# Kernel optimization log

Hardware: AMD Instinct MI355X
Metric: run time of the kernel (lower is better)

Reference implementation:

```python
import jax, jax.numpy as jnp
import numpy as np

N_CHANNELS = 29
HIDDEN = [5, 4, 4]
IN_FEAT = 7
OUT_FEAT = 3
EPS = 1e-07


def _glorot(key, fan_in, fan_out, shape):
    lim = np.sqrt(6.0 / (fan_in + fan_out))
    return jax.random.uniform(key, shape, jnp.float32, -lim, lim)


def _make_params(key):
    # Batched per-channel weights: stack n_channels tiny MLPs along leading dim.
    sizes = [IN_FEAT] + HIDDEN + [OUT_FEAT]
    Ws, bs = [], []
    for i in range(len(sizes) - 1):
        key, k = jax.random.split(key)
        Ws.append(_glorot(k, sizes[i], sizes[i + 1], (N_CHANNELS, sizes[i], sizes[i + 1])))
        bs.append(jnp.zeros((N_CHANNELS, sizes[i + 1]), jnp.float32))
    return Ws, bs


def setup_inputs() -> dict:
    key = jax.random.key(0)
    ks = jax.random.split(key, 16)
    N = 262144
    inp = {
        "tau": jax.random.uniform(ks[0], (N, N_CHANNELS, 1), jnp.float32),
        "mu": jax.random.uniform(ks[1], (N, 1), jnp.float32, 0.05, 1.0),
        "mu_bar": jax.random.uniform(ks[2], (N, 1), jnp.float32, 0.05, 1.0),
        "lw": jax.random.uniform(ks[3], (N, 1), jnp.float32),
        "h2o": jax.random.uniform(ks[4], (N, 1), jnp.float32),
        "o3": jax.random.uniform(ks[5], (N, 1), jnp.float32),
        "co2": jax.random.uniform(ks[6], (N, 1), jnp.float32),
        "u": jax.random.uniform(ks[7], (N, 1), jnp.float32),
        "n2o": jax.random.uniform(ks[8], (N, 1), jnp.float32),
        "ch4": jax.random.uniform(ks[9], (N, 1), jnp.float32),
    }
    Wd, bd = _make_params(ks[10])
    Wf, bf = _make_params(ks[11])
    for i in range(4):
        inp[f"Wd{i}"] = Wd[i]
        inp[f"bd{i}"] = bd[i]
        inp[f"Wf{i}"] = Wf[i]
        inp[f"bf{i}"] = bf[i]
    return inp


def _mlp(x, Ws, bs):
    # x: [N, F]; Ws[i]: [C, fin, fout]; output [N, C, 3]
    h = jnp.einsum('nf,cfh->nch', x, Ws[0]) + bs[0]
    h = jax.nn.relu(h)
    for i in (1, 2):
        h = jnp.einsum('nch,chk->nck', h, Ws[i]) + bs[i]
        h = jax.nn.relu(h)
    h = jnp.einsum('nch,chk->nck', h, Ws[3]) + bs[3]
    return jax.nn.softmax(h, axis=-1)


def reference(tau, mu, mu_bar, lw, h2o, o3, co2, u, n2o, ch4,
              Wd0, bd0, Wd1, bd1, Wd2, bd2, Wd3, bd3,
              Wf0, bf0, Wf1, bf1, Wf2, bf2, Wf3, bf3):
    constituents = jnp.concatenate([lw, h2o, o3, co2, u, n2o, ch4], axis=1)  # [N,7]
    c_direct = constituents / (mu + EPS)
    c_diffuse = constituents / (mu_bar + EPS)
    mu3 = mu[:, :, None]          # [N,1,1]
    mu_bar3 = mu_bar[:, :, None]
    tau_total = jnp.sum(tau, axis=-1, keepdims=True)  # [N,C,1]
    t_direct = jnp.exp(-tau_total / (mu3 + EPS))       # [N,C,1]
    t_diffuse = jnp.exp(-tau_total / (mu_bar3 + EPS))
    e_direct = _mlp(c_direct, [Wd0, Wd1, Wd2, Wd3], [bd0, bd1, bd2, bd3])    # [N,C,3]
    e_diffuse = _mlp(c_diffuse, [Wf0, Wf1, Wf2, Wf3], [bf0, bf1, bf2, bf3])  # [N,C,3]
    return jnp.concatenate([t_direct, t_diffuse, e_direct, e_diffuse], axis=2)  # [N,C,8]
```

## Files before the change

### kernel.cpp

```cpp
#include <hip/hip_runtime.h>

#define EPS 1e-7f
#define NCH 29
#define SPB 128
#define ROWF4 59


typedef float f32x2 __attribute__((ext_vector_type(2)));

__device__ __forceinline__ f32x2 splat2(float v) { f32x2 r; r.x = v; r.y = v; return r; }
__device__ __forceinline__ f32x2 fma2(f32x2 a, f32x2 b, f32x2 c) {
    return __builtin_elementwise_fma(a, b, c);
}
__device__ __forceinline__ f32x2 max2(f32x2 a, f32x2 b) {
    return __builtin_elementwise_max(a, b);
}
__device__ __forceinline__ f32x2 expc2(f32x2 a) {
    f32x2 r; r.x = __expf(a.x); r.y = __expf(a.y); return r;
}
__device__ __forceinline__ f32x2 rcp2(f32x2 a) {
    f32x2 r; r.x = __builtin_amdgcn_rcpf(a.x); r.y = __builtin_amdgcn_rcpf(a.y); return r;
}

__device__ __forceinline__ void barrier_lds_only() {
    asm volatile("s_waitcnt lgkmcnt(0)\n\ts_barrier" ::: "memory");
}

__device__ __forceinline__ void mlp7p(const f32x2 x[7],
    const float* __restrict__ W0, const float* __restrict__ b0,
    const float* __restrict__ W1, const float* __restrict__ b1,
    const float* __restrict__ W2, const float* __restrict__ b2,
    const float* __restrict__ W3, const float* __restrict__ b3,
    f32x2 e[3])
{
    const f32x2 zero = splat2(0.0f);
    f32x2 h0[5];
#pragma unroll
    for (int h = 0; h < 5; ++h) {
        f32x2 a = splat2(b0[h]);
#pragma unroll
        for (int f = 0; f < 7; ++f) a = fma2(x[f], splat2(W0[f * 5 + h]), a);
        h0[h] = max2(a, zero);
    }
    f32x2 h1[4];
#pragma unroll
    for (int k = 0; k < 4; ++k) {
        f32x2 a = splat2(b1[k]);
#pragma unroll
        for (int h = 0; h < 5; ++h) a = fma2(h0[h], splat2(W1[h * 4 + k]), a);
        h1[k] = max2(a, zero);
    }
    f32x2 h2[4];
#pragma unroll
    for (int k = 0; k < 4; ++k) {
        f32x2 a = splat2(b2[k]);
#pragma unroll
        for (int h = 0; h < 4; ++h) a = fma2(h1[h], splat2(W2[h * 4 + k]), a);
        h2[k] = max2(a, zero);
    }
    f32x2 l[3];
#pragma unroll
    for (int k = 0; k < 3; ++k) {
        f32x2 a = splat2(b3[k]);
#pragma unroll
        for (int h = 0; h < 4; ++h) a = fma2(h2[h], splat2(W3[h * 3 + k]), a);
        l[k] = a;
    }
    f32x2 m = max2(l[0], max2(l[1], l[2]));
    f32x2 e0 = expc2(l[0] - m);
    f32x2 e1 = expc2(l[1] - m);
    f32x2 e2 = expc2(l[2] - m);
    f32x2 rs = rcp2(e0 + e1 + e2);
    e[0] = e0 * rs; e[1] = e1 * rs; e[2] = e2 * rs;
}

__global__ __launch_bounds__(512, 4) void lps_kernel(
    const float* __restrict__ tau, const float* __restrict__ mu, const float* __restrict__ mu_bar,
    const float* __restrict__ lw, const float* __restrict__ h2o, const float* __restrict__ o3,
    const float* __restrict__ co2, const float* __restrict__ uu, const float* __restrict__ n2o,
    const float* __restrict__ ch4,
    const float* __restrict__ Wd0, const float* __restrict__ bd0,
    const float* __restrict__ Wf0, const float* __restrict__ bf0,
    const float* __restrict__ Wd1, const float* __restrict__ bd1,
    const float* __restrict__ Wf1, const float* __restrict__ bf1,
    const float* __restrict__ Wd2, const float* __restrict__ bd2,
    const float* __restrict__ Wf2, const float* __restrict__ bf2,
    const float* __restrict__ Wd3, const float* __restrict__ bd3,
    const float* __restrict__ Wf3, const float* __restrict__ bf3,
    float* __restrict__ out, int N)
{
    __shared__ __align__(16) float4 obuf[64 * ROWF4];

    const int tid  = threadIdx.x;
    const int lane = tid & 63;
    const int wid  = __builtin_amdgcn_readfirstlane(tid >> 6);

    const long long base = (long long)blockIdx.x * SPB;
    const int s0 = (int)base + lane;
    const int s1 = s0 + 64;
    const int i0 = (s0 < N) ? s0 : (N - 1);
    const int i1 = (s1 < N) ? s1 : (N - 1);

    f32x2 mu2, mub2;
    mu2.x  = mu[i0];      mu2.y  = mu[i1];
    mub2.x = mu_bar[i0];  mub2.y = mu_bar[i1];
    const f32x2 rmu2   = rcp2(mu2 + splat2(EPS));
    const f32x2 rmub2  = rcp2(mub2 + splat2(EPS));
    const f32x2 nrmu2  = -rmu2;
    const f32x2 nrmub2 = -rmub2;

    f32x2 cons2[7];
    cons2[0].x = lw[i0];  cons2[0].y = lw[i1];
    cons2[1].x = h2o[i0]; cons2[1].y = h2o[i1];
    cons2[2].x = o3[i0];  cons2[2].y = o3[i1];
    cons2[3].x = co2[i0]; cons2[3].y = co2[i1];
    cons2[4].x = uu[i0];  cons2[4].y = uu[i1];
    cons2[5].x = n2o[i0]; cons2[5].y = n2o[i1];
    cons2[6].x = ch4[i0]; cons2[6].y = ch4[i1];

    f32x2 x2d[7], x2f[7];
#pragma unroll
    for (int f = 0; f < 7; ++f) { x2d[f] = cons2[f] * rmu2; x2f[f] = cons2[f] * rmub2; }

    float ry[4][8];

#pragma unroll
    for (int it = 0; it < 4; ++it) {
        const int c = wid + it * 8;
        if (c < NCH) {
            f32x2 tau2;
            tau2.x = tau[(size_t)i0 * NCH + c];
            tau2.y = tau[(size_t)i1 * NCH + c];
            f32x2 td2 = expc2(tau2 * nrmu2);
            f32x2 tf2 = expc2(tau2 * nrmub2);

            f32x2 ed[3], ef[3];
            mlp7p(x2d, Wd0 + c * 35, bd0 + c * 5, Wd1 + c * 20, bd1 + c * 4,
                       Wd2 + c * 16, bd2 + c * 4, Wd3 + c * 12, bd3 + c * 3, ed);
            mlp7p(x2f, Wf0 + c * 35, bf0 + c * 5, Wf1 + c * 20, bf1 + c * 4,
                       Wf2 + c * 16, bf2 + c * 4, Wf3 + c * 12, bf3 + c * 3, ef);

            obuf[lane * ROWF4 + c * 2]     = make_float4(td2.x, tf2.x, ed[0].x, ed[1].x);
            obuf[lane * ROWF4 + c * 2 + 1] = make_float4(ed[2].x, ef[0].x, ef[1].x, ef[2].x);
            ry[it][0] = td2.y;   ry[it][1] = tf2.y;
            ry[it][2] = ed[0].y; ry[it][3] = ed[1].y;
            ry[it][4] = ed[2].y; ry[it][5] = ef[0].y;
            ry[it][6] = ef[1].y; ry[it][7] = ef[2].y;
        }
    }

    float4* out4 = (float4*)out;

    barrier_lds_only();
    {
        int n0 = N - (int)base; n0 = (n0 > 64) ? 64 : n0;
        if (n0 > 0) {
            const int tot = n0 * 58;
            const long long ob = base * 58;
            for (int i = tid; i < tot; i += 512) {
                const int s = i / 58, r = i - s * 58;
                out4[ob + i] = obuf[s * ROWF4 + r];
            }
        }
    }
    barrier_lds_only();

#pragma unroll
    for (int it = 0; it < 4; ++it) {
        const int c = wid + it * 8;
        if (c < NCH) {
            obuf[lane * ROWF4 + c * 2]     = make_float4(ry[it][0], ry[it][1], ry[it][2], ry[it][3]);
            obuf[lane * ROWF4 + c * 2 + 1] = make_float4(ry[it][4], ry[it][5], ry[it][6], ry[it][7]);
        }
    }
    barrier_lds_only();

    {
        int n1 = N - (int)base - 64; n1 = (n1 > 64) ? 64 : n1;
        if (n1 > 0) {
            const int tot = n1 * 58;
            const long long ob = (base + 64) * 58;
            for (int i = tid; i < tot; i += 512) {
                const int s = i / 58, r = i - s * 58;
                out4[ob + i] = obuf[s * ROWF4 + r];
            }
        }
    }
}

extern "C" void kernel_launch(void* const* d_in, const int* in_sizes, int n_in,
                              void* d_out, int out_size, void* d_ws, size_t ws_size,
                              hipStream_t stream) {
    const float* tau    = (const float*)d_in[0];
    const float* mu     = (const float*)d_in[1];
    const float* mu_bar = (const float*)d_in[2];
    const float* lw     = (const float*)d_in[3];
    const float* h2o    = (const float*)d_in[4];
    const float* o3     = (const float*)d_in[5];
    const float* co2    = (const float*)d_in[6];
    const float* uu     = (const float*)d_in[7];
    const float* n2o    = (const float*)d_in[8];
    const float* ch4    = (const float*)d_in[9];

    const float* Wd0 = (const float*)d_in[10];
    const float* bd0 = (const float*)d_in[11];
    const float* Wf0 = (const float*)d_in[12];
    const float* bf0 = (const float*)d_in[13];
    const float* Wd1 = (const float*)d_in[14];
    const float* bd1 = (const float*)d_in[15];
    const float* Wf1 = (const float*)d_in[16];
    const float* bf1 = (const float*)d_in[17];
    const float* Wd2 = (const float*)d_in[18];
    const float* bd2 = (const float*)d_in[19];
    const float* Wf2 = (const float*)d_in[20];
    const float* bf2 = (const float*)d_in[21];
    const float* Wd3 = (const float*)d_in[22];
    const float* bd3 = (const float*)d_in[23];
    const float* Wf3 = (const float*)d_in[24];
    const float* bf3 = (const float*)d_in[25];

    float* out = (float*)d_out;
    int N = in_sizes[1];

    int blocks = (N + SPB - 1) / SPB;
    lps_kernel<<<blocks, 512, 0, stream>>>(
        tau, mu, mu_bar, lw, h2o, o3, co2, uu, n2o, ch4,
        Wd0, bd0, Wf0, bf0, Wd1, bd1, Wf1, bf1,
        Wd2, bd2, Wf2, bf2, Wd3, bd3, Wf3, bf3,
        out, N);
}
```

Measured before the change: 82.72 us.

## Stream output per channel group through smaller LDS buffer with interleaved stores

Replaces the two-phase output staging, which kept both samples' results in registers and then drained a full 64-sample buffer twice, with a per-channel-group loop. Each iteration writes all 128 samples for 8 channels into a small LDS buffer and flushes it straight to global memory. The aim is to shrink LDS use and register pressure (the ry array goes away) and to overlap global stores with the compute of later channel groups. The cost is eight barriers instead of three, and each store pass writes 256-byte row chunks rather than fully contiguous spans.

```diff
diff --git a/kernel.cpp b/kernel.cpp
--- a/kernel.cpp
+++ b/kernel.cpp
@@ -3,7 +3,7 @@
 #define EPS 1e-7f
 #define NCH 29
 #define SPB 128
-#define ROWF4 59
+#define ROWA 17
 
 
 typedef float f32x2 __attribute__((ext_vector_type(2)));
@@ -89,7 +89,7 @@
     const float* __restrict__ Wf3, const float* __restrict__ bf3,
     float* __restrict__ out, int N)
 {
-    __shared__ __align__(16) float4 obuf[64 * ROWF4];
+    __shared__ __align__(16) float4 obuf[SPB * ROWA];
 
     const int tid  = threadIdx.x;
     const int lane = tid & 63;
@@ -109,30 +109,31 @@
     const f32x2 nrmu2  = -rmu2;
     const f32x2 nrmub2 = -rmub2;
 
-    f32x2 cons2[7];
-    cons2[0].x = lw[i0];  cons2[0].y = lw[i1];
-    cons2[1].x = h2o[i0]; cons2[1].y = h2o[i1];
-    cons2[2].x = o3[i0];  cons2[2].y = o3[i1];
-    cons2[3].x = co2[i0]; cons2[3].y = co2[i1];
-    cons2[4].x = uu[i0];  cons2[4].y = uu[i1];
-    cons2[5].x = n2o[i0]; cons2[5].y = n2o[i1];
-    cons2[6].x = ch4[i0]; cons2[6].y = ch4[i1];
-
     f32x2 x2d[7], x2f[7];
-#pragma unroll
-    for (int f = 0; f < 7; ++f) { x2d[f] = cons2[f] * rmu2; x2f[f] = cons2[f] * rmub2; }
-
-    float ry[4][8];
-
-#pragma unroll
-    for (int it = 0; it < 4; ++it) {
-        const int c = wid + it * 8;
+    {
+        f32x2 t;
+        t.x = lw[i0];  t.y = lw[i1];  x2d[0] = t * rmu2; x2f[0] = t * rmub2;
+        t.x = h2o[i0]; t.y = h2o[i1]; x2d[1] = t * rmu2; x2f[1] = t * rmub2;
+        t.x = o3[i0];  t.y = o3[i1];  x2d[2] = t * rmu2; x2f[2] = t * rmub2;
+        t.x = co2[i0]; t.y = co2[i1]; x2d[3] = t * rmu2; x2f[3] = t * rmub2;
+        t.x = uu[i0];  t.y = uu[i1];  x2d[4] = t * rmu2; x2f[4] = t * rmub2;
+        t.x = n2o[i0]; t.y = n2o[i1]; x2d[5] = t * rmu2; x2f[5] = t * rmub2;
+        t.x = ch4[i0]; t.y = ch4[i1]; x2d[6] = t * rmu2; x2f[6] = t * rmub2;
+    }
+
+    int nsamp = N - (int)base;
+    if (nsamp > SPB) nsamp = SPB;
+    float4* out4 = (float4*)out;
+
+#pragma unroll
+    for (int k = 0; k < 4; ++k) {
+        const int c = k * 8 + wid;
         if (c < NCH) {
             f32x2 tau2;
             tau2.x = tau[(size_t)i0 * NCH + c];
             tau2.y = tau[(size_t)i1 * NCH + c];
-            f32x2 td2 = expc2(tau2 * nrmu2);
-            f32x2 tf2 = expc2(tau2 * nrmub2);
+            const f32x2 td2 = expc2(tau2 * nrmu2);
+            const f32x2 tf2 = expc2(tau2 * nrmub2);
 
             f32x2 ed[3], ef[3];
             mlp7p(x2d, Wd0 + c * 35, bd0 + c * 5, Wd1 + c * 20, bd1 + c * 4,
@@ -140,51 +141,32 @@
             mlp7p(x2f, Wf0 + c * 35, bf0 + c * 5, Wf1 + c * 20, bf1 + c * 4,
                        Wf2 + c * 16, bf2 + c * 4, Wf3 + c * 12, bf3 + c * 3, ef);
 
-            obuf[lane * ROWF4 + c * 2]     = make_float4(td2.x, tf2.x, ed[0].x, ed[1].x);
-            obuf[lane * ROWF4 + c * 2 + 1] = make_float4(ed[2].x, ef[0].x, ef[1].x, ef[2].x);
-            ry[it][0] = td2.y;   ry[it][1] = tf2.y;
-            ry[it][2] = ed[0].y; ry[it][3] = ed[1].y;
-            ry[it][4] = ed[2].y; ry[it][5] = ef[0].y;
-            ry[it][6] = ef[1].y; ry[it][7] = ef[2].y;
+            const int r = (c - k * 8) * 2;
+            obuf[lane * ROWA + r]            = make_float4(td2.x, tf2.x, ed[0].x, ed[1].x);
+            obuf[lane * ROWA + r + 1]        = make_float4(ed[2].x, ef[0].x, ef[1].x, ef[2].x);
+            obuf[(lane + 64) * ROWA + r]     = make_float4(td2.y, tf2.y, ed[0].y, ed[1].y);
+            obuf[(lane + 64) * ROWA + r + 1] = make_float4(ed[2].y, ef[0].y, ef[1].y, ef[2].y);
         }
-    }
-
-    float4* out4 = (float4*)out;
-
-    barrier_lds_only();
-    {
-        int n0 = N - (int)base; n0 = (n0 > 64) ? 64 : n0;
-        if (n0 > 0) {
-            const int tot = n0 * 58;
-            const long long ob = base * 58;
-            for (int i = tid; i < tot; i += 512) {
-                const int s = i / 58, r = i - s * 58;
-                out4[ob + i] = obuf[s * ROWF4 + r];
+
+        barrier_lds_only();
+
+        if (nsamp > 0) {
+            if (k < 3) {
+                const int tot = nsamp * 16;
+                for (int i = tid; i < tot; i += 512) {
+                    const int s = i >> 4, rr = i & 15;
+                    out4[(base + s) * 58 + k * 16 + rr] = obuf[s * ROWA + rr];
+                }
+            } else {
+                const int tot = nsamp * 10;
+                for (int i = tid; i < tot; i += 512) {
+                    const int s = i / 10, rr = i - s * 10;
+                    out4[(base + s) * 58 + 48 + rr] = obuf[s * ROWA + rr];
+                }
             }
         }
-    }
-    barrier_lds_only();
-
-#pragma unroll
-    for (int it = 0; it < 4; ++it) {
-        const int c = wid + it * 8;
-        if (c < NCH) {
-            obuf[lane * ROWF4 + c * 2]     = make_float4(ry[it][0], ry[it][1], ry[it][2], ry[it][3]);
-            obuf[lane * ROWF4 + c * 2 + 1] = make_float4(ry[it][4], ry[it][5], ry[it][6], ry[it][7]);
-        }
-    }
-    barrier_lds_only();
-
-    {
-        int n1 = N - (int)base - 64; n1 = (n1 > 64) ? 64 : n1;
-        if (n1 > 0) {
-            const int tot = n1 * 58;
-            const long long ob = (base + 64) * 58;
-            for (int i = tid; i < tot; i += 512) {
-                const int s = i / 58, r = i - s * 58;
-                out4[ob + i] = obuf[s * ROWF4 + r];
-            }
-        }
+
+        barrier_lds_only();
     }
 }
 
```

Measured after the change: 81.38 us. About the same (-1.6%).
